# Kernel tuning notes

Hardware: AMD Instinct MI355X
Metric: run time of the kernel (lower is better)

Reference implementation:

```python
import jax, jax.numpy as jnp
import numpy as np

N = 4096        # sequence length
H = 16          # heads
D_MODEL = 1024
D_HEAD = D_MODEL // H  # 64


def setup_inputs() -> dict:
    key = jax.random.key(0)
    ks = jax.random.split(key, 9)
    scale = 1.0 / np.sqrt(D_MODEL)
    inp = {
        "X_Q": jax.random.normal(ks[0], (N, D_MODEL), dtype=jnp.float32),
        "X_K": jax.random.normal(ks[1], (N, D_MODEL), dtype=jnp.float32),
        "X_V": jax.random.normal(ks[2], (N, D_MODEL), dtype=jnp.float32),
        # per-head projection weights, stacked over head axis: [H, D_MODEL, D_HEAD]
        "Wq": jax.random.normal(ks[3], (H, D_MODEL, D_HEAD), dtype=jnp.float32) * scale,
        "bq": jax.random.normal(ks[4], (H, D_HEAD), dtype=jnp.float32) * scale,
        "Wk": jax.random.normal(ks[5], (H, D_MODEL, D_HEAD), dtype=jnp.float32) * scale,
        "bk": jax.random.normal(ks[6], (H, D_HEAD), dtype=jnp.float32) * scale,
        "Wv": jax.random.normal(ks[7], (H, D_MODEL, D_HEAD), dtype=jnp.float32) * scale,
        "bv": jax.random.normal(ks[8], (H, D_HEAD), dtype=jnp.float32) * scale,
    }
    return inp


def reference(X_Q, X_K, X_V, Wq, bq, Wk, bk, Wv, bv):
    # Batched per-head projections (replaces the Python loop of nn.Linear calls)
    Q = jnp.einsum("nd,hdk->hnk", X_Q, Wq) + bq[:, None, :]   # [H, N, D_HEAD]
    K = jnp.einsum("nd,hdk->hnk", X_K, Wk) + bk[:, None, :]
    V = jnp.einsum("nd,hdk->hnk", X_V, Wv) + bv[:, None, :]
    scores = jnp.einsum("hnk,hmk->hnm", Q, K) / jnp.sqrt(jnp.float32(D_HEAD))  # [H, N, N]
    attn = jax.nn.softmax(scores, axis=-1)  # softmax over keys (dim=1 of the [n,n] per-head matrix)
    out = jnp.einsum("hnm,hmv->hnv", attn, V)  # [H, N, D_HEAD]
    # concat heads along feature dim -> [N, D_MODEL]
    return jnp.transpose(out, (1, 0, 2)).reshape(N, D_MODEL)
```

## Files before the change

### kernel.cpp

```cpp
#include <hip/hip_runtime.h>

typedef unsigned short u16;
typedef __attribute__((ext_vector_type(8))) short bf16x8;
typedef __attribute__((ext_vector_type(16))) float floatx16;

#define C2 0.18033688011112042f
#define TRUNC_BIAS 0.99859f

static __device__ __forceinline__ u16 f2b(float f) {
  unsigned u = __builtin_bit_cast(unsigned, f);
  u = (u + 0x7FFFu + ((u >> 16) & 1u)) >> 16;
  return (u16)u;
}
static __device__ __forceinline__ unsigned pk2(float a, float b) {
  return (unsigned)f2b(a) | ((unsigned)f2b(b) << 16);
}
static __device__ __forceinline__ void gl_lds16(const void* g, void* l) {
  __builtin_amdgcn_global_load_lds(
      (const __attribute__((address_space(1))) unsigned*)g,
      (__attribute__((address_space(3))) unsigned*)l, 16, 0, 0);
}
static __device__ __forceinline__ float ex2(float x) {
#if __has_builtin(__builtin_amdgcn_exp2f)
  return __builtin_amdgcn_exp2f(x);
#else
  return exp2f(x);
#endif
}
static __device__ __forceinline__ unsigned pkt(float a, float b) {
#if __has_builtin(__builtin_amdgcn_perm)
  return __builtin_amdgcn_perm(__builtin_bit_cast(unsigned, a),
                               __builtin_bit_cast(unsigned, b), 0x03020706u);
#else
  return (__builtin_bit_cast(unsigned, a) >> 16) |
         (__builtin_bit_cast(unsigned, b) & 0xffff0000u);
#endif
}
static __device__ __forceinline__ void pswap(unsigned& a, unsigned& b) {
#if __has_builtin(__builtin_amdgcn_permlane32_swap)
  auto r = __builtin_amdgcn_permlane32_swap(a, b, false, false);
  a = r[0];
  b = r[1];
#else
  unsigned ta = (unsigned)__shfl_xor((int)a, 32);
  unsigned tb = (unsigned)__shfl_xor((int)b, 32);
  bool hi = (threadIdx.x & 32) != 0;
  unsigned na = hi ? tb : a;
  unsigned nb = hi ? b : ta;
  a = na;
  b = nb;
#endif
}

__global__ __launch_bounds__(256) void convx_k(
    const float* __restrict__ x0, const float* __restrict__ x1, const float* __restrict__ x2,
    u16* __restrict__ o0, u16* __restrict__ o1, u16* __restrict__ o2) {
  int z = blockIdx.z;
  const float* x = z == 0 ? x0 : (z == 1 ? x1 : x2);
  u16* o = z == 0 ? o0 : (z == 1 ? o1 : o2);
  size_t i = ((size_t)blockIdx.x * 256 + threadIdx.x) * 8;
  float4 a = *(const float4*)(x + i);
  float4 b = *(const float4*)(x + i + 4);
  uint4 u;
  u.x = pk2(a.x, a.y); u.y = pk2(a.z, a.w);
  u.z = pk2(b.x, b.y); u.w = pk2(b.z, b.w);
  *(uint4*)(o + i) = u;
}

__global__ __launch_bounds__(256) void convw_k(
    const float* __restrict__ w0, const float* __restrict__ w1, const float* __restrict__ w2,
    u16* __restrict__ o0, u16* __restrict__ o1, u16* __restrict__ o2) {
  int z = blockIdx.z;
  const float* W = z == 0 ? w0 : (z == 1 ? w1 : w2);
  u16* O = z == 0 ? o0 : (z == 1 ? o1 : o2);
  int h = blockIdx.x >> 4, d0 = (blockIdx.x & 15) * 64;
  __shared__ __align__(16) float tile[64 * 68];
  int t = threadIdx.x;
  {
    int r = t >> 2, c = t & 3;
    const float* src = W + (size_t)h * 65536 + (size_t)(d0 + r) * 64 + c * 16;
#pragma unroll
    for (int i = 0; i < 4; ++i) {
      float4 v = *(const float4*)(src + 4 * i);
      *(float4*)&tile[r * 68 + c * 16 + 4 * i] = v;
    }
  }
  __syncthreads();
  {
    int k = t >> 2, dc = t & 3;
    unsigned u[8];
#pragma unroll
    for (int i = 0; i < 8; ++i) {
      float a = tile[(dc * 16 + 2 * i) * 68 + k];
      float b = tile[(dc * 16 + 2 * i + 1) * 68 + k];
      u[i] = pk2(a, b);
    }
    u16* dst = O + ((size_t)(h * 64 + k)) * 1024 + d0 + dc * 16;
    *(uint4*)dst = make_uint4(u[0], u[1], u[2], u[3]);
    *(uint4*)(dst + 8) = make_uint4(u[4], u[5], u[6], u[7]);
  }
}

__global__ __launch_bounds__(256, 3) void proj_k(
    const u16* __restrict__ x0, const u16* __restrict__ x1, const u16* __restrict__ x2,
    const u16* __restrict__ w0, const u16* __restrict__ w1, const u16* __restrict__ w2,
    const float* __restrict__ b0, const float* __restrict__ b1, const float* __restrict__ b2,
    u16* __restrict__ q0, u16* __restrict__ q1, u16* __restrict__ q2) {
  int z = blockIdx.z;
  const u16* X = z == 0 ? x0 : (z == 1 ? x1 : x2);
  const u16* Wt = z == 0 ? w0 : (z == 1 ? w1 : w2);
  const float* bias = z == 0 ? b0 : (z == 1 ? b1 : b2);
  u16* out = z == 0 ? q0 : (z == 1 ? q1 : q2);
  const float osc = (z == 0) ? C2 : 1.0f;

  __shared__ uint4 smem4[16384 / 16];
  char* sm = (char*)smem4;
  const int t = threadIdx.x, lane = t & 63, wid = t >> 6;
  const int L = lane & 31, h2 = lane >> 5;
  const int wm = wid >> 1, wc = wid & 1;
  const int rowt = blockIdx.x + 8 * (blockIdx.y & 3);
  const int colt = blockIdx.y >> 2;
  const int n0 = rowt * 128, c0 = colt * 128;

  floatx16 acc[2][2];
#pragma unroll
  for (int a = 0; a < 2; ++a)
#pragma unroll
    for (int b = 0; b < 2; ++b)
#pragma unroll
      for (int r = 0; r < 16; ++r) acc[a][b][r] = 0.f;

  const int srow = t >> 2, sc = t & 3;
  for (int k0 = 0; k0 < 1024; k0 += 32) {
#pragma unroll
    for (int i = 0; i < 2; ++i) {
      int row = i * 64 + srow;
      int cg = sc ^ ((row >> 1) & 3);
      gl_lds16(X + (size_t)(n0 + row) * 1024 + k0 + cg * 8, sm + i * 4096 + wid * 1024);
    }
#pragma unroll
    for (int i = 0; i < 2; ++i) {
      int row = i * 64 + srow;
      int cg = sc ^ ((row >> 1) & 3);
      gl_lds16(Wt + (size_t)(c0 + row) * 1024 + k0 + cg * 8, sm + 8192 + i * 4096 + wid * 1024);
    }
    __syncthreads();
#pragma unroll
    for (int ks = 0; ks < 2; ++ks) {
      bf16x8 af[2], bfr[2];
#pragma unroll
      for (int mt = 0; mt < 2; ++mt) {
        int m = wm * 64 + mt * 32 + L;
        int cc = (2 * ks + h2) ^ ((m >> 1) & 3);
        af[mt] = *(const bf16x8*)(sm + m * 64 + cc * 16);
      }
#pragma unroll
      for (int ct = 0; ct < 2; ++ct) {
        int c = wc * 64 + ct * 32 + L;
        int cc = (2 * ks + h2) ^ ((c >> 1) & 3);
        bfr[ct] = *(const bf16x8*)(sm + 8192 + c * 64 + cc * 16);
      }
#pragma unroll
      for (int mt = 0; mt < 2; ++mt)
#pragma unroll
        for (int ct = 0; ct < 2; ++ct)
          acc[mt][ct] = __builtin_amdgcn_mfma_f32_32x32x16_bf16(af[mt], bfr[ct], acc[mt][ct], 0, 0, 0);
    }
    __syncthreads();
  }
#pragma unroll
  for (int ct = 0; ct < 2; ++ct) {
    int gcol = c0 + wc * 64 + ct * 32 + L;
    float bv = bias[gcol];
    int h = gcol >> 6, cl = gcol & 63;
#pragma unroll
    for (int mt = 0; mt < 2; ++mt)
#pragma unroll
      for (int r = 0; r < 16; ++r) {
        int seq = n0 + wm * 64 + mt * 32 + (r & 3) + 8 * (r >> 2) + 4 * h2;
        out[((size_t)h * 4096 + seq) * 64 + cl] = f2b((acc[mt][ct][r] + bv) * osc);
      }
  }
}

__global__ __launch_bounds__(256) void kpack_k(const u16* __restrict__ Kin, u16* __restrict__ Kp) {
  int o = blockIdx.x * 256 + threadIdx.x;
  int l = o & 63;
  int rest = o >> 6;
  int ks = rest & 3;
  int hT = rest >> 2;
  int n = ((hT & 127) << 5) | (l & 31);
  int h = hT >> 7;
  int d8 = ks * 2 + (l >> 5);
  uint4 v = *(const uint4*)(Kin + (((size_t)h * 4096 + n) << 6) + d8 * 8);
  *(uint4*)(Kp + ((size_t)o << 3)) = v;
}

__global__ __launch_bounds__(256) void vpack_k(const u16* __restrict__ V, u16* __restrict__ Vp) {
  int h = blockIdx.x & 15, nb = blockIdx.x >> 4;
  __shared__ __align__(16) u16 tile[64 * 72];
  int t = threadIdx.x;
  {
    int r = t >> 2, c = t & 3;
    const u16* src = V + ((size_t)(h * 4096 + nb * 64 + r)) * 64 + c * 16;
    *(bf16x8*)&tile[r * 72 + c * 16] = *(const bf16x8*)src;
    *(bf16x8*)&tile[r * 72 + c * 16 + 8] = *(const bf16x8*)(src + 8);
  }
  __syncthreads();
  u16* Vph = Vp + (size_t)h * 262144;
  {
    int v = t >> 2, nc = t & 3;
    unsigned u[8];
#pragma unroll
    for (int i = 0; i < 8; ++i) {
      unsigned lo = tile[(nc * 16 + 2 * i) * 72 + v];
      unsigned hi = tile[(nc * 16 + 2 * i + 1) * 72 + v];
      u[i] = lo | (hi << 16);
    }
    int vt = v >> 5, L = v & 31;
#pragma unroll
    for (int half = 0; half < 2; ++half) {
      int c = nb * 8 + nc * 2 + half;
      int T = c >> 2, c2 = (c >> 1) & 1, h2c = c & 1;
      uint4 wv = half == 0 ? make_uint4(u[0], u[1], u[2], u[3])
                           : make_uint4(u[4], u[5], u[6], u[7]);
      *(uint4*)(Vph + (((size_t)(T * 4 + vt * 2 + c2) * 64 + h2c * 32 + L) << 3)) = wv;
    }
  }
}

__global__ __launch_bounds__(512, 2) void attn_k(
    const u16* __restrict__ Q, const u16* __restrict__ Kp, const u16* __restrict__ Vp,
    float* __restrict__ out) {
  __shared__ __align__(16) float Ob[4][64 * 68];
  __shared__ float lstat[8][64];
  const int t = threadIdx.x, lane = t & 63, w = t >> 6;
  const int L = lane & 31, h2 = lane >> 5;
  const int ws = w & 3, kh = w >> 2;
  const int h = blockIdx.x & 15, qt = blockIdx.x >> 4;
  const int n0 = qt * 256 + ws * 64;
  const u16* Qg = Q + (size_t)h * 4096 * 64;
  const u16* Kph = Kp + (size_t)h * 262144;
  const u16* Vph = Vp + (size_t)h * 262144;
  const int tbase = kh * 64;

  bf16x8 qf[2][4];
#pragma unroll
  for (int nt = 0; nt < 2; ++nt)
#pragma unroll
    for (int ks = 0; ks < 4; ++ks)
      qf[nt][ks] = *(const bf16x8*)(Qg + ((size_t)(n0 + nt * 32 + L)) * 64 + ks * 16 + h2 * 8);

  const floatx16 FZ = {0.f, 0.f, 0.f, 0.f, 0.f, 0.f, 0.f, 0.f,
                       0.f, 0.f, 0.f, 0.f, 0.f, 0.f, 0.f, 0.f};
  floatx16 accO[2][2];
#pragma unroll
  for (int a = 0; a < 2; ++a)
#pragma unroll
    for (int b = 0; b < 2; ++b) accO[a][b] = FZ;
  float l_run[2] = {0.f, 0.f};

  bf16x8 kfA[4], kfB[4], vfA[4], vfB[4];
  auto loadK = [&](int rn, bf16x8* kf) {
    const u16* p = Kph + ((size_t)(tbase + rn) << 11) + lane * 8;
#pragma unroll
    for (int ks = 0; ks < 4; ++ks) kf[ks] = *(const bf16x8*)(p + ks * 512);
  };
  auto loadV = [&](int rn, bf16x8* vf) {
    const u16* p = Vph + ((size_t)(tbase + rn) << 11) + lane * 8;
#pragma unroll
    for (int idx = 0; idx < 4; ++idx) vf[idx] = *(const bf16x8*)(p + idx * 512);
  };
  loadK(0, kfA);
  loadV(0, vfA);

  auto round = [&](int r, bf16x8* kf, bf16x8* vf, bf16x8* kfn, bf16x8* vfn) {
    floatx16 accS[2];
    accS[0] = __builtin_amdgcn_mfma_f32_32x32x16_bf16(kf[0], qf[0][0], FZ, 0, 0, 0);
    accS[1] = __builtin_amdgcn_mfma_f32_32x32x16_bf16(kf[0], qf[1][0], FZ, 0, 0, 0);
#pragma unroll
    for (int ks = 1; ks < 4; ++ks) {
      accS[0] = __builtin_amdgcn_mfma_f32_32x32x16_bf16(kf[ks], qf[0][ks], accS[0], 0, 0, 0);
      accS[1] = __builtin_amdgcn_mfma_f32_32x32x16_bf16(kf[ks], qf[1][ks], accS[1], 0, 0, 0);
    }
    int rn = (r + 1) & 63;
    loadK(rn, kfn);
    loadV(rn, vfn);

    unsigned pkr[2][8];
#pragma unroll
    for (int nt = 0; nt < 2; ++nt) {
      float p[16];
      float ss = 0.f;
#pragma unroll
      for (int q = 0; q < 16; ++q) {
        p[q] = ex2(accS[nt][q]);
        ss += p[q];
      }
      l_run[nt] += ss;
#pragma unroll
      for (int g = 0; g < 8; ++g) pkr[nt][g] = pkt(p[2 * g], p[2 * g + 1]);
      pswap(pkr[nt][0], pkr[nt][2]);
      pswap(pkr[nt][1], pkr[nt][3]);
      pswap(pkr[nt][4], pkr[nt][6]);
      pswap(pkr[nt][5], pkr[nt][7]);
    }

#pragma unroll
    for (int c2 = 0; c2 < 2; ++c2) {
      bf16x8 pf[2];
#pragma unroll
      for (int nt = 0; nt < 2; ++nt) {
        uint4 u = make_uint4(pkr[nt][c2 * 4], pkr[nt][c2 * 4 + 1],
                             pkr[nt][c2 * 4 + 2], pkr[nt][c2 * 4 + 3]);
        pf[nt] = __builtin_bit_cast(bf16x8, u);
      }
#pragma unroll
      for (int vt = 0; vt < 2; ++vt) {
        accO[vt][0] = __builtin_amdgcn_mfma_f32_32x32x16_bf16(vf[vt * 2 + c2], pf[0], accO[vt][0], 0, 0, 0);
        accO[vt][1] = __builtin_amdgcn_mfma_f32_32x32x16_bf16(vf[vt * 2 + c2], pf[1], accO[vt][1], 0, 0, 0);
      }
    }
  };

  for (int r = 0; r < 64; r += 2) {
    round(r, kfA, vfA, kfB, vfB);
    round(r + 1, kfB, vfB, kfA, vfA);
  }

  l_run[0] += __shfl_xor(l_run[0], 32);
  l_run[1] += __shfl_xor(l_run[1], 32);
  if (h2 == 0) {
    lstat[w][L] = l_run[0];
    lstat[w][32 + L] = l_run[1];
  }
  if (kh == 1) {
#pragma unroll
    for (int vt = 0; vt < 2; ++vt)
#pragma unroll
      for (int nt = 0; nt < 2; ++nt)
#pragma unroll
        for (int g = 0; g < 4; ++g)
          *(float4*)&Ob[ws][(nt * 32 + L) * 68 + vt * 32 + 8 * g + 4 * h2] =
              make_float4(accO[vt][nt][4 * g], accO[vt][nt][4 * g + 1],
                          accO[vt][nt][4 * g + 2], accO[vt][nt][4 * g + 3]);
  }
  __syncthreads();
  if (kh == 0) {
    float scale[2];
#pragma unroll
    for (int nt = 0; nt < 2; ++nt)
      scale[nt] = 1.f / ((lstat[w][nt * 32 + L] + lstat[w + 4][nt * 32 + L]) * TRUNC_BIAS);
#pragma unroll
    for (int vt = 0; vt < 2; ++vt)
#pragma unroll
      for (int nt = 0; nt < 2; ++nt)
#pragma unroll
        for (int g = 0; g < 4; ++g) {
          float4 o = *(const float4*)&Ob[ws][(nt * 32 + L) * 68 + vt * 32 + 8 * g + 4 * h2];
          float4 res;
          res.x = (accO[vt][nt][4 * g] + o.x) * scale[nt];
          res.y = (accO[vt][nt][4 * g + 1] + o.y) * scale[nt];
          res.z = (accO[vt][nt][4 * g + 2] + o.z) * scale[nt];
          res.w = (accO[vt][nt][4 * g + 3] + o.w) * scale[nt];
          *(float4*)(out + ((size_t)(n0 + nt * 32 + L)) * 1024 + h * 64 + vt * 32 + 8 * g + 4 * h2) = res;
        }
  }
}

extern "C" void kernel_launch(void* const* d_in, const int* in_sizes, int n_in,
                              void* d_out, int out_size, void* d_ws, size_t ws_size,
                              hipStream_t stream) {
  const float* XQ = (const float*)d_in[0];
  const float* XK = (const float*)d_in[1];
  const float* XV = (const float*)d_in[2];
  const float* Wq = (const float*)d_in[3];
  const float* bq = (const float*)d_in[4];
  const float* Wk = (const float*)d_in[5];
  const float* bk = (const float*)d_in[6];
  const float* Wv = (const float*)d_in[7];
  const float* bv = (const float*)d_in[8];

  const size_t MB = 1024 * 1024;
  char* w = (char*)d_ws;
  u16* xqb = (u16*)(w + 0 * MB);
  u16* xkb = (u16*)(w + 8 * MB);
  u16* xvb = (u16*)(w + 16 * MB);
  u16* wtq = (u16*)(w + 24 * MB);
  u16* wtk = (u16*)(w + 26 * MB);
  u16* wtv = (u16*)(w + 28 * MB);
  u16* Qb = (u16*)(w + 32 * MB);
  u16* Kb = (u16*)(w + 40 * MB);
  u16* Vb = (u16*)(w + 48 * MB);
  u16* Kpk = (u16*)(w + 56 * MB);
  u16* Vpk = (u16*)(w + 64 * MB);

  convx_k<<<dim3(2048, 1, 3), 256, 0, stream>>>(XQ, XK, XV, xqb, xkb, xvb);
  convw_k<<<dim3(256, 1, 3), 256, 0, stream>>>(Wq, Wk, Wv, wtq, wtk, wtv);
  proj_k<<<dim3(8, 32, 3), 256, 0, stream>>>(xqb, xkb, xvb, wtq, wtk, wtv,
                                             bq, bk, bv, Qb, Kb, Vb);
  kpack_k<<<dim3(4096), 256, 0, stream>>>(Kb, Kpk);
  vpack_k<<<dim3(1024), 256, 0, stream>>>(Vb, Vpk);
  attn_k<<<dim3(256), 512, 0, stream>>>(Qb, Kpk, Vpk, (float*)d_out);
}
```

Measured before the change: 223.9 us.

## Software-pipeline QK and PV MFMAs across key rounds with priority hints

Restructures the attention inner loop so that the QK MFMAs of round r are issued together with the PV MFMAs of round r-1. The exp and pack work of round r then runs after the next K/V fragment loads are issued, and s_setprio raises wave priority around the matrix-core block. The goal is to hide the exp/pack and load latency behind tensor-core work instead of running them back to back. The row-sum of the exponentials is rewritten as a tree reduction to shorten the dependency chain. In exchange, the loop gains a prologue and epilogue, one redundant final K/V load, and higher register pressure from keeping accS and pkr live across stages.

```diff
diff --git a/kernel.cpp b/kernel.cpp
--- a/kernel.cpp
+++ b/kernel.cpp
@@ -260,6 +260,8 @@
     for (int b = 0; b < 2; ++b) accO[a][b] = FZ;
   float l_run[2] = {0.f, 0.f};
 
+  floatx16 accS[2];
+  unsigned pkr[2][8];
   bf16x8 kfA[4], kfB[4], vfA[4], vfB[4];
   auto loadK = [&](int rn, bf16x8* kf) {
     const u16* p = Kph + ((size_t)(tbase + rn) << 11) + lane * 8;
@@ -271,11 +273,8 @@
 #pragma unroll
     for (int idx = 0; idx < 4; ++idx) vf[idx] = *(const bf16x8*)(p + idx * 512);
   };
-  loadK(0, kfA);
-  loadV(0, vfA);
-
-  auto round = [&](int r, bf16x8* kf, bf16x8* vf, bf16x8* kfn, bf16x8* vfn) {
-    floatx16 accS[2];
+
+  auto qk = [&](bf16x8* kf) {
     accS[0] = __builtin_amdgcn_mfma_f32_32x32x16_bf16(kf[0], qf[0][0], FZ, 0, 0, 0);
     accS[1] = __builtin_amdgcn_mfma_f32_32x32x16_bf16(kf[0], qf[1][0], FZ, 0, 0, 0);
 #pragma unroll
@@ -283,21 +282,35 @@
       accS[0] = __builtin_amdgcn_mfma_f32_32x32x16_bf16(kf[ks], qf[0][ks], accS[0], 0, 0, 0);
       accS[1] = __builtin_amdgcn_mfma_f32_32x32x16_bf16(kf[ks], qf[1][ks], accS[1], 0, 0, 0);
     }
-    int rn = (r + 1) & 63;
-    loadK(rn, kfn);
-    loadV(rn, vfn);
-
-    unsigned pkr[2][8];
+  };
+  auto pv = [&](bf16x8* vf) {
+#pragma unroll
+    for (int c2 = 0; c2 < 2; ++c2) {
+      bf16x8 pf[2];
+#pragma unroll
+      for (int nt = 0; nt < 2; ++nt) {
+        uint4 u = make_uint4(pkr[nt][c2 * 4], pkr[nt][c2 * 4 + 1],
+                             pkr[nt][c2 * 4 + 2], pkr[nt][c2 * 4 + 3]);
+        pf[nt] = __builtin_bit_cast(bf16x8, u);
+      }
+#pragma unroll
+      for (int vt = 0; vt < 2; ++vt) {
+        accO[vt][0] = __builtin_amdgcn_mfma_f32_32x32x16_bf16(vf[vt * 2 + c2], pf[0], accO[vt][0], 0, 0, 0);
+        accO[vt][1] = __builtin_amdgcn_mfma_f32_32x32x16_bf16(vf[vt * 2 + c2], pf[1], accO[vt][1], 0, 0, 0);
+      }
+    }
+  };
+  auto expack = [&]() {
 #pragma unroll
     for (int nt = 0; nt < 2; ++nt) {
       float p[16];
-      float ss = 0.f;
-#pragma unroll
-      for (int q = 0; q < 16; ++q) {
-        p[q] = ex2(accS[nt][q]);
-        ss += p[q];
-      }
-      l_run[nt] += ss;
+#pragma unroll
+      for (int q = 0; q < 16; ++q) p[q] = ex2(accS[nt][q]);
+      float s0 = (p[0] + p[1]) + (p[2] + p[3]);
+      float s1 = (p[4] + p[5]) + (p[6] + p[7]);
+      float s2 = (p[8] + p[9]) + (p[10] + p[11]);
+      float s3 = (p[12] + p[13]) + (p[14] + p[15]);
+      l_run[nt] += (s0 + s1) + (s2 + s3);
 #pragma unroll
       for (int g = 0; g < 8; ++g) pkr[nt][g] = pkt(p[2 * g], p[2 * g + 1]);
       pswap(pkr[nt][0], pkr[nt][2]);
@@ -305,28 +318,32 @@
       pswap(pkr[nt][4], pkr[nt][6]);
       pswap(pkr[nt][5], pkr[nt][7]);
     }
-
-#pragma unroll
-    for (int c2 = 0; c2 < 2; ++c2) {
-      bf16x8 pf[2];
-#pragma unroll
-      for (int nt = 0; nt < 2; ++nt) {
-        uint4 u = make_uint4(pkr[nt][c2 * 4], pkr[nt][c2 * 4 + 1],
-                             pkr[nt][c2 * 4 + 2], pkr[nt][c2 * 4 + 3]);
-        pf[nt] = __builtin_bit_cast(bf16x8, u);
-      }
-#pragma unroll
-      for (int vt = 0; vt < 2; ++vt) {
-        accO[vt][0] = __builtin_amdgcn_mfma_f32_32x32x16_bf16(vf[vt * 2 + c2], pf[0], accO[vt][0], 0, 0, 0);
-        accO[vt][1] = __builtin_amdgcn_mfma_f32_32x32x16_bf16(vf[vt * 2 + c2], pf[1], accO[vt][1], 0, 0, 0);
-      }
-    }
-  };
-
-  for (int r = 0; r < 64; r += 2) {
-    round(r, kfA, vfA, kfB, vfB);
-    round(r + 1, kfB, vfB, kfA, vfA);
-  }
+  };
+
+  auto pipe = [&](int r, bf16x8* kc, bf16x8* kn, bf16x8* vn) {
+    __builtin_amdgcn_s_setprio(1);
+    qk(kc);
+    pv(vn);
+    __builtin_amdgcn_s_setprio(0);
+    int rn = (r + 1) & 63;
+    loadK(rn, kn);
+    loadV(rn, vn);
+    expack();
+  };
+
+  loadK(0, kfA);
+  loadV(0, vfA);
+  qk(kfA);
+  loadK(1, kfB);
+  loadV(1, vfB);
+  expack();
+
+  for (int r = 1; r < 63; r += 2) {
+    pipe(r, kfB, kfA, vfA);
+    pipe(r + 1, kfA, kfB, vfB);
+  }
+  pipe(63, kfB, kfA, vfA);
+  pv(vfB);
 
   l_run[0] += __shfl_xor(l_run[0], 32);
   l_run[1] += __shfl_xor(l_run[1], 32);
```

Measured after the change: 236.9 us. +5.8%, slower.

## Split attention key range four ways per block, doubling grid to 512 blocks

Applied to the files above, without the earlier changes.

Each block now handles 128 query rows with 2 wave groups of rows and 4-way key splitting, instead of 256 rows with 4 row groups and 2-way key split. The grid doubles to 512 blocks, so the 256 CUs are filled more evenly, and launch bounds ask for 4 blocks per CU. The price is a two-stage LDS reduction of partial outputs with extra barriers and a tighter register budget, which may cause spills.

```diff
diff --git a/kernel.cpp b/kernel.cpp
--- a/kernel.cpp
+++ b/kernel.cpp
@@ -229,20 +229,20 @@
   }
 }
 
-__global__ __launch_bounds__(512, 2) void attn_k(
+__global__ __launch_bounds__(512, 4) void attn_k(
     const u16* __restrict__ Q, const u16* __restrict__ Kp, const u16* __restrict__ Vp,
     float* __restrict__ out) {
-  __shared__ __align__(16) float Ob[4][64 * 68];
+  __shared__ __align__(16) float Ob[2][2][64 * 68];
   __shared__ float lstat[8][64];
   const int t = threadIdx.x, lane = t & 63, w = t >> 6;
   const int L = lane & 31, h2 = lane >> 5;
-  const int ws = w & 3, kh = w >> 2;
+  const int ws = w & 1, kh = w >> 1;
   const int h = blockIdx.x & 15, qt = blockIdx.x >> 4;
-  const int n0 = qt * 256 + ws * 64;
+  const int n0 = qt * 128 + ws * 64;
   const u16* Qg = Q + (size_t)h * 4096 * 64;
   const u16* Kph = Kp + (size_t)h * 262144;
   const u16* Vph = Vp + (size_t)h * 262144;
-  const int tbase = kh * 64;
+  const int tbase = kh * 32;
 
   bf16x8 qf[2][4];
 #pragma unroll
@@ -283,7 +283,7 @@
       accS[0] = __builtin_amdgcn_mfma_f32_32x32x16_bf16(kf[ks], qf[0][ks], accS[0], 0, 0, 0);
       accS[1] = __builtin_amdgcn_mfma_f32_32x32x16_bf16(kf[ks], qf[1][ks], accS[1], 0, 0, 0);
     }
-    int rn = (r + 1) & 63;
+    int rn = (r + 1) & 31;
     loadK(rn, kfn);
     loadV(rn, vfn);
 
@@ -323,7 +323,7 @@
     }
   };
 
-  for (int r = 0; r < 64; r += 2) {
+  for (int r = 0; r < 32; r += 2) {
     round(r, kfA, vfA, kfB, vfB);
     round(r + 1, kfB, vfB, kfA, vfA);
   }
@@ -334,6 +334,33 @@
     lstat[w][L] = l_run[0];
     lstat[w][32 + L] = l_run[1];
   }
+  if (kh >= 2) {
+#pragma unroll
+    for (int vt = 0; vt < 2; ++vt)
+#pragma unroll
+      for (int nt = 0; nt < 2; ++nt)
+#pragma unroll
+        for (int g = 0; g < 4; ++g)
+          *(float4*)&Ob[ws][kh - 2][(nt * 32 + L) * 68 + vt * 32 + 8 * g + 4 * h2] =
+              make_float4(accO[vt][nt][4 * g], accO[vt][nt][4 * g + 1],
+                          accO[vt][nt][4 * g + 2], accO[vt][nt][4 * g + 3]);
+  }
+  __syncthreads();
+  if (kh < 2) {
+#pragma unroll
+    for (int vt = 0; vt < 2; ++vt)
+#pragma unroll
+      for (int nt = 0; nt < 2; ++nt)
+#pragma unroll
+        for (int g = 0; g < 4; ++g) {
+          float4 o = *(const float4*)&Ob[ws][kh][(nt * 32 + L) * 68 + vt * 32 + 8 * g + 4 * h2];
+          accO[vt][nt][4 * g] += o.x;
+          accO[vt][nt][4 * g + 1] += o.y;
+          accO[vt][nt][4 * g + 2] += o.z;
+          accO[vt][nt][4 * g + 3] += o.w;
+        }
+  }
+  __syncthreads();
   if (kh == 1) {
 #pragma unroll
     for (int vt = 0; vt < 2; ++vt)
@@ -341,7 +368,7 @@
       for (int nt = 0; nt < 2; ++nt)
 #pragma unroll
         for (int g = 0; g < 4; ++g)
-          *(float4*)&Ob[ws][(nt * 32 + L) * 68 + vt * 32 + 8 * g + 4 * h2] =
+          *(float4*)&Ob[ws][0][(nt * 32 + L) * 68 + vt * 32 + 8 * g + 4 * h2] =
               make_float4(accO[vt][nt][4 * g], accO[vt][nt][4 * g + 1],
                           accO[vt][nt][4 * g + 2], accO[vt][nt][4 * g + 3]);
   }
@@ -350,14 +377,16 @@
     float scale[2];
 #pragma unroll
     for (int nt = 0; nt < 2; ++nt)
-      scale[nt] = 1.f / ((lstat[w][nt * 32 + L] + lstat[w + 4][nt * 32 + L]) * TRUNC_BIAS);
+      scale[nt] = 1.f / ((lstat[ws][nt * 32 + L] + lstat[ws + 2][nt * 32 + L] +
+                          lstat[ws + 4][nt * 32 + L] + lstat[ws + 6][nt * 32 + L]) *
+                         TRUNC_BIAS);
 #pragma unroll
     for (int vt = 0; vt < 2; ++vt)
 #pragma unroll
       for (int nt = 0; nt < 2; ++nt)
 #pragma unroll
         for (int g = 0; g < 4; ++g) {
-          float4 o = *(const float4*)&Ob[ws][(nt * 32 + L) * 68 + vt * 32 + 8 * g + 4 * h2];
+          float4 o = *(const float4*)&Ob[ws][0][(nt * 32 + L) * 68 + vt * 32 + 8 * g + 4 * h2];
           float4 res;
           res.x = (accO[vt][nt][4 * g] + o.x) * scale[nt];
           res.y = (accO[vt][nt][4 * g + 1] + o.y) * scale[nt];
@@ -401,5 +430,5 @@
                                              bq, bk, bv, Qb, Kb, Vb);
   kpack_k<<<dim3(4096), 256, 0, stream>>>(Kb, Kpk);
   vpack_k<<<dim3(1024), 256, 0, stream>>>(Vb, Vpk);
-  attn_k<<<dim3(256), 512, 0, stream>>>(Qb, Kpk, Vpk, (float*)d_out);
-}
+  attn_k<<<dim3(512), 512, 0, stream>>>(Qb, Kpk, Vpk, (float*)d_out);
+}
```

After: 483.7 us. +116.0%, slower.
